# Performance work log

Hardware: AMD Instinct MI355X
Metric: run time of the kernel (lower is better)

Reference implementation:

```python
import jax, jax.numpy as jnp
import numpy as np

N_HEAD = 16
N_KV_HEAD = 4
N_EMBD = 2048

def rotate_half(x):
    x1, x2 = jnp.split(x, 2, axis=-1)
    return jnp.concatenate([-x2, x1], axis=-1)

def rope_tables(T, k):
    # angles = 10000^(-2*i/k) for i in [0, k/2); cos/sin repeated twice along last dim
    inv = jnp.power(10000.0, -2.0 * jnp.arange(k // 2, dtype=jnp.float32) / k)
    ang = jnp.arange(T, dtype=jnp.float32)[:, None] * inv[None, :]  # [T, k/2]
    cos = jnp.tile(jnp.cos(ang), (1, 2))  # [T, k]
    sin = jnp.tile(jnp.sin(ang), (1, 2))
    return cos, sin

def setup_inputs() -> dict:
    key = jax.random.key(0)
    ks = jax.random.split(key, 5)
    B, T, D = 4, 1024, N_EMBD
    g, h = N_KV_HEAD, N_HEAD
    k = D // h
    s = 0.02
    return {
        'x': jax.random.normal(ks[0], (B, T, D), dtype=jnp.float32),
        'Wq': jax.random.normal(ks[1], (D, D), dtype=jnp.float32) * s,
        'Wk': jax.random.normal(ks[2], (D, g * k), dtype=jnp.float32) * s,
        'Wv': jax.random.normal(ks[3], (D, g * k), dtype=jnp.float32) * s,
        'Wo': jax.random.normal(ks[4], (D, D), dtype=jnp.float32) * s,
    }

def reference(x, Wq, Wk, Wv, Wo):
    B, T, D = x.shape
    h, g = N_HEAD, N_KV_HEAD
    k = D // h
    Q = (x @ Wq).reshape(B, T, h, k).transpose(0, 2, 1, 3)  # [B,h,T,k]
    K = (x @ Wk).reshape(B, T, g, k).transpose(0, 2, 1, 3)  # [B,g,T,k]
    V = (x @ Wv).reshape(B, T, g, k).transpose(0, 2, 1, 3)
    # GQA: repeat_interleave kv heads to match query heads
    K = jnp.repeat(K, h // g, axis=1)  # [B,h,T,k]
    V = jnp.repeat(V, h // g, axis=1)
    cos, sin = rope_tables(T, k)
    cos = cos[None, None]  # [1,1,T,k]
    sin = sin[None, None]
    Q = Q * cos + rotate_half(Q) * sin
    K = K * cos + rotate_half(K) * sin
    scores = jnp.einsum('bhqk,bhsk->bhqs', Q, K) / jnp.sqrt(jnp.float32(k))
    causal = jnp.tril(jnp.ones((T, T), dtype=bool))
    scores = jnp.where(causal[None, None], scores, -jnp.inf)
    A = jax.nn.softmax(scores, axis=-1)
    Y = jnp.einsum('bhqs,bhsk->bhqk', A, V)
    Y = Y.transpose(0, 2, 1, 3).reshape(B, T, D)
    return Y @ Wo
```

## Files before the change

kernel.cpp:

```cpp
#include <hip/hip_runtime.h>
#include <math.h>

#define B_ 4
#define T_ 1024
#define D_ 2048
#define NH 16
#define NKV 4
#define HD 128
#define KV_D 512
#define QKV_S 2560

typedef __attribute__((ext_vector_type(8))) short short8;
typedef __attribute__((ext_vector_type(4))) float f32x4;

__device__ __forceinline__ ushort f2b(float f) {
    unsigned u = __float_as_uint(f);
    return (ushort)((u + 0x7fffu + ((u >> 16) & 1u)) >> 16);
}
__device__ __forceinline__ float b2f(ushort u) {
    return __uint_as_float((unsigned)u << 16);
}

#if __has_builtin(__builtin_amdgcn_exp2f)
#define EXP2F(x) __builtin_amdgcn_exp2f(x)
#else
#define EXP2F(x) __expf((x) * 0.6931471805599453f)
#endif

#define ASYNC_COPY16(g, l)                                                  \
    __builtin_amdgcn_global_load_lds(                                       \
        (const __attribute__((address_space(1))) void*)(g),                 \
        (__attribute__((address_space(3))) void*)(l), 16, 0, 0)

#define SCHED0() __builtin_amdgcn_sched_barrier(0)
#define SBAR() __builtin_amdgcn_s_barrier()
#define WAITV0() asm volatile("s_waitcnt vmcnt(0)" ::: "memory")
#define MFMA16(ap, bp, cc) cc = __builtin_amdgcn_mfma_f32_16x16x32_bf16(ap, bp, cc, 0, 0, 0)

__global__ __launch_bounds__(256) void prep_all(const float* __restrict__ x,
                                                const float* __restrict__ Wq,
                                                const float* __restrict__ Wk,
                                                const float* __restrict__ Wv,
                                                const float* __restrict__ Wo,
                                                ushort* __restrict__ xb,
                                                ushort* __restrict__ WqkvT,
                                                ushort* __restrict__ WoT,
                                                float2* __restrict__ tab) {
    __shared__ float tile[32][33];
    const int bid = blockIdx.x;
    if (bid < 8192) {
        const int i = bid * 256 + threadIdx.x;
        const float4 v = ((const float4*)x)[i];
        ushort4 u;
        u.x = f2b(v.x); u.y = f2b(v.y); u.z = f2b(v.z); u.w = f2b(v.w);
        ((ushort4*)xb)[i] = u;
        return;
    }
    if (bid >= 18432) {
        const int idx = (bid - 18432) * 256 + threadIdx.x;
        const int t = idx >> 6, i = idx & 63;
        const float inv = exp2f((float)i * (-13.287712379549449f / 64.0f));
        const float ang = (float)t * inv;
        tab[idx] = make_float2(cosf(ang), sinf(ang));
        return;
    }
    const float* W;
    ushort* WT;
    int N, rb;
    if (bid < 12288)      { W = Wq; WT = WqkvT;                           N = D_;   rb = bid - 8192; }
    else if (bid < 13312) { W = Wk; WT = WqkvT + (size_t)D_ * D_;         N = KV_D; rb = bid - 12288; }
    else if (bid < 14336) { W = Wv; WT = WqkvT + (size_t)(D_+KV_D) * D_;  N = KV_D; rb = bid - 13312; }
    else                  { W = Wo; WT = WoT;                             N = D_;   rb = bid - 14336; }
    const int bxn = N / 32;
    const int n0 = (rb % bxn) * 32, k0 = (rb / bxn) * 32;
    const int tx = threadIdx.x & 31, ty = threadIdx.x >> 5;
    for (int i = ty; i < 32; i += 8)
        tile[i][tx] = W[(size_t)(k0 + i) * N + n0 + tx];
    __syncthreads();
    for (int i = ty; i < 32; i += 8)
        WT[(size_t)(n0 + i) * D_ + k0 + tx] = f2b(tile[tx][i]);
}

__global__ __launch_bounds__(512, 2) void gemm_qkv256(const ushort* __restrict__ A,
                                                      const ushort* __restrict__ BT,
                                                      ushort* __restrict__ QKV,
                                                      ushort* __restrict__ Vt,
                                                      const float2* __restrict__ tab) {
    extern __shared__ ushort smem[];
    const int K = D_;
    const int NT = K / 64;
    const int tid = threadIdx.x;
    const int m0 = blockIdx.y * 256, n0 = blockIdx.x * 256;
    const int wave = tid >> 6, lane = tid & 63;
    const int wr = wave >> 2, wc = wave & 3;
    const int ln = lane & 15, quad = lane >> 4;

    const int rl = tid >> 3;
    const int cus = ((tid & 7) * 8) ^ ((rl & 7) << 3);
    const ushort* Ag = A + (size_t)(m0 + rl) * K + cus;
    const ushort* Bg = BT + (size_t)(n0 + rl) * K + cus;
    ushort* const stA = smem + tid * 8;
    ushort* const stB = smem + 32768 + tid * 8;

    const int cq0 = (quad * 8) ^ ((ln & 7) << 3);
    const int abase0 = wr * 8192 + ln * 64;
    const int bbase0 = 32768 + (wc >> 1) * 8192 + ((wc & 1) * 64 + ln) * 64;

    f32x4 acc[8][4];
    const f32x4 zero = {0.f, 0.f, 0.f, 0.f};
#pragma unroll
    for (int i = 0; i < 8; ++i)
#pragma unroll
        for (int j = 0; j < 4; ++j) acc[i][j] = zero;

    short8 a[4][2], b0[2][2], b1[2][2];

#define GLOADS(dnoff, koff)                                                 \
    do {                                                                    \
        const ushort* Agk = Ag + (koff);                                    \
        const ushort* Bgk = Bg + (koff);                                    \
        ASYNC_COPY16(Agk,                    stA + (dnoff));                \
        ASYNC_COPY16(Agk + (size_t)64 * K,   stA + (dnoff) + 4096);         \
        ASYNC_COPY16(Agk + (size_t)128 * K,  stA + (dnoff) + 8192);         \
        ASYNC_COPY16(Agk + (size_t)192 * K,  stA + (dnoff) + 12288);        \
        ASYNC_COPY16(Bgk,                    stB + (dnoff));                \
        ASYNC_COPY16(Bgk + (size_t)64 * K,   stB + (dnoff) + 4096);         \
        ASYNC_COPY16(Bgk + (size_t)128 * K,  stB + (dnoff) + 8192);         \
        ASYNC_COPY16(Bgk + (size_t)192 * K,  stB + (dnoff) + 12288);        \
    } while (0)

#define READ_A(dst, base, roff)                                             \
    _Pragma("unroll")                                                       \
    for (int mt = 0; mt < 4; ++mt) {                                        \
        dst[mt][0] = *(const short8*)&smem[(base) + (roff) + mt * 1024 + cq0];        \
        dst[mt][1] = *(const short8*)&smem[(base) + (roff) + mt * 1024 + (cq0 ^ 32)]; \
    }
#define READ_B(dst, base, noff)                                             \
    _Pragma("unroll")                                                       \
    for (int nt = 0; nt < 2; ++nt) {                                        \
        dst[nt][0] = *(const short8*)&smem[(base) + (noff) + nt * 1024 + cq0];        \
        dst[nt][1] = *(const short8*)&smem[(base) + (noff) + nt * 1024 + (cq0 ^ 32)]; \
    }
#define QUAD_MMA(ar, br, mo, no)                                            \
    _Pragma("unroll")                                                       \
    for (int mt = 0; mt < 4; ++mt)                                          \
        _Pragma("unroll")                                                   \
        for (int nt = 0; nt < 2; ++nt) {                                    \
            MFMA16(ar[mt][0], br[nt][0], acc[(mo) + mt][(no) + nt]);        \
            MFMA16(ar[mt][1], br[nt][1], acc[(mo) + mt][(no) + nt]);        \
        }

    GLOADS(0, 0);
    WAITV0();
    SBAR();
    SCHED0();
    READ_A(a, abase0, 0);
    READ_B(b0, bbase0, 0);

#pragma unroll 1
    for (int t = 0; t < NT; ++t) {
        const int cb = (t & 1) * 16384;
        const int nb = cb ^ 16384;
        const bool more = (t + 1) < NT;

        READ_B(b1, bbase0 + cb, 2048);
        if (more) GLOADS(nb, (t + 1) * 64);
        SCHED0();
        SBAR();
        __builtin_amdgcn_s_setprio(1);
        QUAD_MMA(a, b0, 0, 0);
        __builtin_amdgcn_s_setprio(0);

        SCHED0();
        SBAR();
        __builtin_amdgcn_s_setprio(1);
        QUAD_MMA(a, b1, 0, 2);
        __builtin_amdgcn_s_setprio(0);

        READ_A(a, abase0 + cb, 4096);
        __builtin_amdgcn_s_setprio(1);
        QUAD_MMA(a, b1, 4, 2);
        __builtin_amdgcn_s_setprio(0);

        if (more) WAITV0();
        SCHED0();
        SBAR();
        SCHED0();
        __builtin_amdgcn_s_setprio(1);
        QUAD_MMA(a, b0, 4, 0);
        __builtin_amdgcn_s_setprio(0);
        if (more) {
            READ_A(a, abase0 + nb, 0);
            READ_B(b0, bbase0 + nb, 0);
        }
    }
#undef GLOADS
#undef READ_A
#undef READ_B
#undef QUAD_MMA

    __syncthreads();
    ushort* Epi = smem;
    const int b = m0 >> 10;
    const int t0 = m0 & 1023;
    const int hid0 = n0 >> 7;

    for (int hh = 0; hh < 2; ++hh) {
        if ((wc >> 1) == hh) {
            const int cb2 = (wc & 1) * 64;
#pragma unroll
            for (int am = 0; am < 8; ++am)
#pragma unroll
                for (int an = 0; an < 4; ++an)
#pragma unroll
                    for (int r = 0; r < 4; ++r)
                        Epi[(wr * 128 + am * 16 + quad * 4 + r) * 136 + cb2 + an * 16 + ln] =
                            f2b(acc[am][an][r]);
        }
        __syncthreads();

        const int hid = hid0 + hh;
        if (hid < NH + NKV) {
            const bool isQ = hid < NH;
            const size_t colbase = isQ ? (size_t)hid * HD : (size_t)D_ + (size_t)(hid - NH) * HD;
            const float sc = isQ ? (0.08838834764831845f * 1.4426950408889634f) : 1.0f;
            const int r = tid >> 1;
            const int hf = tid & 1;
            const int tt = t0 + r;
            ushort* orow = QKV + (size_t)(m0 + r) * QKV_S + colbase;
            const float4* tab4 = (const float4*)tab;
#pragma unroll
            for (int jj = 0; jj < 4; ++jj) {
                const int dbase = hf * 32 + jj * 8;
                const short8 lo = *(const short8*)&Epi[r * 136 + dbase];
                const short8 hi = *(const short8*)&Epi[r * 136 + 64 + dbase];
                ushort olo[8], ohi[8];
#pragma unroll
                for (int kq = 0; kq < 4; ++kq) {
                    const float4 cs = tab4[((tt * 64 + dbase) >> 1) + kq];
                    const float x1a = b2f(lo[2 * kq]),     x2a = b2f(hi[2 * kq]);
                    const float x1b = b2f(lo[2 * kq + 1]), x2b = b2f(hi[2 * kq + 1]);
                    olo[2 * kq]     = f2b((x1a * cs.x - x2a * cs.y) * sc);
                    ohi[2 * kq]     = f2b((x2a * cs.x + x1a * cs.y) * sc);
                    olo[2 * kq + 1] = f2b((x1b * cs.z - x2b * cs.w) * sc);
                    ohi[2 * kq + 1] = f2b((x2b * cs.z + x1b * cs.w) * sc);
                }
                *(short8*)&orow[dbase]      = *(short8*)olo;
                *(short8*)&orow[dbase + 64] = *(short8*)ohi;
            }
        } else {
            const int kv = hid - (NH + NKV);
            const int dd = tid & 127;
            const int th = tid >> 7;
            ushort* vrow = Vt + ((size_t)((b * NKV + kv) * HD + dd)) * T_ + t0 + th * 64;
#pragma unroll
            for (int jj = 0; jj < 8; ++jj) {
                ushort pk[8];
#pragma unroll
                for (int k2 = 0; k2 < 8; ++k2)
                    pk[k2] = Epi[(th * 64 + jj * 8 + k2) * 136 + dd];
                *(short8*)&vrow[jj * 8] = *(short8*)pk;
            }
        }
        __syncthreads();
    }
}

__global__ __launch_bounds__(256) void gemm_bf16(const ushort* __restrict__ A,
                                                 const ushort* __restrict__ BT,
                                                 float* __restrict__ C,
                                                 int M, int N, int K) {
    __shared__ ushort As[128 * 32];
    __shared__ ushort Bs[128 * 32];
    const int tid = threadIdx.x;
    const int m0 = blockIdx.y * 128, n0 = blockIdx.x * 128;
    const int wave = tid >> 6, lane = tid & 63;
    const int wm = (wave >> 1) * 64, wn = (wave & 1) * 64;
    const int lrow = lane & 15;
    const int quad = lane >> 4;

    f32x4 acc[4][4];
    const f32x4 zero = {0.f, 0.f, 0.f, 0.f};
#pragma unroll
    for (int i = 0; i < 4; ++i)
#pragma unroll
        for (int j = 0; j < 4; ++j) acc[i][j] = zero;

    const int srow = tid >> 2;
    const int scol = (tid & 3) * 8;
    const ushort* Ag = A + (size_t)(m0 + srow) * K + scol;
    const ushort* Bg = BT + (size_t)(n0 + srow) * K + scol;
    ushort* AsT = As + tid * 8;
    ushort* BsT = Bs + tid * 8;

    for (int k0 = 0; k0 < K; k0 += 32) {
        ASYNC_COPY16(Ag + k0, AsT);
        ASYNC_COPY16(Ag + k0 + (size_t)64 * K, AsT + 64 * 32);
        ASYNC_COPY16(Bg + k0, BsT);
        ASYNC_COPY16(Bg + k0 + (size_t)64 * K, BsT + 64 * 32);
        __syncthreads();

        short8 a[4], b[4];
#pragma unroll
        for (int mt = 0; mt < 4; ++mt)
            a[mt] = *(const short8*)&As[(wm + mt * 16 + lrow) * 32 + quad * 8];
#pragma unroll
        for (int nt = 0; nt < 4; ++nt)
            b[nt] = *(const short8*)&Bs[(wn + nt * 16 + lrow) * 32 + quad * 8];
#pragma unroll
        for (int mt = 0; mt < 4; ++mt)
#pragma unroll
            for (int nt = 0; nt < 4; ++nt)
                acc[mt][nt] = __builtin_amdgcn_mfma_f32_16x16x32_bf16(
                    a[mt], b[nt], acc[mt][nt], 0, 0, 0);
        __syncthreads();
    }

    const int crow = quad * 4;
    const int ccol = lrow;
#pragma unroll
    for (int mt = 0; mt < 4; ++mt)
#pragma unroll
        for (int nt = 0; nt < 4; ++nt)
#pragma unroll
            for (int r = 0; r < 4; ++r)
                C[(size_t)(m0 + wm + mt * 16 + crow + r) * N +
                  n0 + wn + nt * 16 + ccol] = acc[mt][nt][r];
}

__global__ __launch_bounds__(256) void attn_mfma(const ushort* __restrict__ QKV,
                                                 const ushort* __restrict__ Vt,
                                                 ushort* __restrict__ Yb) {
    __shared__ ushort Ks[64][136];
    __shared__ ushort Vs[128][72];
    __shared__ ushort Ps[4][16][72];

    const int bh = blockIdx.x;
    const int qt = (int)gridDim.y - 1 - (int)blockIdx.y;
    const int b = bh >> 4, h = bh & 15;
    const int kvh = h >> 2;
    const int q0 = qt * 64;
    const int tid = threadIdx.x;
    const int wave = tid >> 6, lane = tid & 63;
    const int ln = lane & 15, quad = lane >> 4;

    short8 qf[4];
    {
        const ushort* qp = QKV + ((size_t)(b * T_ + q0 + wave * 16 + ln)) * QKV_S + h * HD + quad * 8;
#pragma unroll
        for (int f = 0; f < 4; ++f) qf[f] = *(const short8*)(qp + f * 32);
    }

    f32x4 acc[8];
    const f32x4 zero = {0.f, 0.f, 0.f, 0.f};
#pragma unroll
    for (int j = 0; j < 8; ++j) acc[j] = zero;
    float m_r[4], l_r[4];
#pragma unroll
    for (int r = 0; r < 4; ++r) { m_r[r] = -INFINITY; l_r[r] = 0.f; }

    const int qrow = q0 + wave * 16 + quad * 4;

    for (int kt = 0; kt <= qt; ++kt) {
        const int s0 = kt * 64;
        __syncthreads();
#pragma unroll
        for (int c = 0; c < 4; ++c) {
            const int cid = tid + 256 * c;
            const int s = cid >> 4, ch = cid & 15;
            *(short8*)&Ks[s][ch * 8] =
                *(const short8*)&QKV[((size_t)(b * T_ + s0 + s)) * QKV_S + D_ + kvh * HD + ch * 8];
        }
#pragma unroll
        for (int c = 0; c < 4; ++c) {
            const int cid = tid + 256 * c;
            const int d = cid >> 3, ch = cid & 7;
            *(short8*)&Vs[d][ch * 8] =
                *(const short8*)&Vt[((size_t)((b * NKV + kvh) * HD + d)) * T_ + s0 + ch * 8];
        }
        __syncthreads();

        float sc[4][4];
#pragma unroll
        for (int ct = 0; ct < 4; ++ct) {
            f32x4 s4 = zero;
#pragma unroll
            for (int f = 0; f < 4; ++f)
                s4 = __builtin_amdgcn_mfma_f32_16x16x32_bf16(
                    qf[f], *(const short8*)&Ks[ct * 16 + ln][f * 32 + quad * 8], s4, 0, 0, 0);
#pragma unroll
            for (int r = 0; r < 4; ++r) sc[ct][r] = s4[r];
        }
        if (kt == qt) {
#pragma unroll
            for (int ct = 0; ct < 4; ++ct)
#pragma unroll
                for (int r = 0; r < 4; ++r)
                    if (s0 + ct * 16 + ln > qrow + r) sc[ct][r] = -INFINITY;
        }
        float alpha[4];
#pragma unroll
        for (int r = 0; r < 4; ++r) {
            float mx = fmaxf(fmaxf(sc[0][r], sc[1][r]), fmaxf(sc[2][r], sc[3][r]));
            mx = fmaxf(mx, __shfl_xor(mx, 1));
            mx = fmaxf(mx, __shfl_xor(mx, 2));
            mx = fmaxf(mx, __shfl_xor(mx, 4));
            mx = fmaxf(mx, __shfl_xor(mx, 8));
            const float mnew = fmaxf(m_r[r], mx);
            alpha[r] = EXP2F(m_r[r] - mnew);
            m_r[r] = mnew;
#pragma unroll
            for (int ct = 0; ct < 4; ++ct) sc[ct][r] = EXP2F(sc[ct][r] - mnew);
            float sum = (sc[0][r] + sc[1][r]) + (sc[2][r] + sc[3][r]);
            sum += __shfl_xor(sum, 1);
            sum += __shfl_xor(sum, 2);
            sum += __shfl_xor(sum, 4);
            sum += __shfl_xor(sum, 8);
            l_r[r] = l_r[r] * alpha[r] + sum;
        }
#pragma unroll
        for (int ct = 0; ct < 4; ++ct)
#pragma unroll
            for (int r = 0; r < 4; ++r)
                Ps[wave][quad * 4 + r][ct * 16 + ln] = f2b(sc[ct][r]);
#pragma unroll
        for (int j = 0; j < 8; ++j)
#pragma unroll
            for (int r = 0; r < 4; ++r) acc[j][r] *= alpha[r];
        const short8 pa0 = *(const short8*)&Ps[wave][ln][quad * 8];
        const short8 pa1 = *(const short8*)&Ps[wave][ln][32 + quad * 8];
#pragma unroll
        for (int j = 0; j < 8; ++j) {
            acc[j] = __builtin_amdgcn_mfma_f32_16x16x32_bf16(
                pa0, *(const short8*)&Vs[j * 16 + ln][quad * 8], acc[j], 0, 0, 0);
            acc[j] = __builtin_amdgcn_mfma_f32_16x16x32_bf16(
                pa1, *(const short8*)&Vs[j * 16 + ln][32 + quad * 8], acc[j], 0, 0, 0);
        }
    }

    float invl[4];
#pragma unroll
    for (int r = 0; r < 4; ++r) invl[r] = 1.f / l_r[r];
    ushort* yb = Yb + ((size_t)(b * T_ + qrow)) * D_ + h * HD + ln;
#pragma unroll
    for (int r = 0; r < 4; ++r)
#pragma unroll
        for (int j = 0; j < 8; ++j)
            yb[(size_t)r * D_ + j * 16] = f2b(acc[j][r] * invl[r]);
}

extern "C" void kernel_launch(void* const* d_in, const int* in_sizes, int n_in,
                              void* d_out, int out_size, void* d_ws, size_t ws_size,
                              hipStream_t stream) {
    const float* x  = (const float*)d_in[0];
    const float* Wq = (const float*)d_in[1];
    const float* Wk = (const float*)d_in[2];
    const float* Wv = (const float*)d_in[3];
    const float* Wo = (const float*)d_in[4];
    float* out = (float*)d_out;

    char* w = (char*)d_ws;
    ushort* xb    = (ushort*)w;  w += (size_t)4096 * D_ * 2;
    ushort* WqkvT = (ushort*)w;  w += (size_t)3072 * D_ * 2;
    ushort* QKV   = (ushort*)w;  w += (size_t)4096 * QKV_S * 2;
    ushort* Vt    = (ushort*)w;  w += (size_t)B_ * KV_D * T_ * 2;
    ushort* Yb    = (ushort*)w;  w += (size_t)4096 * D_ * 2;
    ushort* WoT   = (ushort*)w;  w += (size_t)D_ * D_ * 2;
    float2* tab   = (float2*)w;  w += (size_t)T_ * 64 * 8;

    const int M = B_ * T_;
    dim3 blk(256);

    hipFuncSetAttribute(reinterpret_cast<const void*>(gemm_qkv256),
                        hipFuncAttributeMaxDynamicSharedMemorySize, 131072);

    prep_all<<<18688, blk, 0, stream>>>(x, Wq, Wk, Wv, Wo, xb, WqkvT, WoT, tab);

    gemm_qkv256<<<dim3(3072 / 256, M / 256), dim3(512), 131072, stream>>>(xb, WqkvT, QKV, Vt, tab);

    attn_mfma<<<dim3(B_ * NH, T_ / 64), blk, 0, stream>>>(QKV, Vt, Yb);

    gemm_bf16<<<dim3(D_ / 128, M / 128), blk, 0, stream>>>(Yb, WoT, out, M, D_, D_);
}
```

Measured before the change: 302.5 us.

## Deepen GEMM global-to-LDS prefetch to two tiles ahead with partial vmcnt waits

Restructures the QKV GEMM main loop so global-to-LDS async copies are issued two K-tiles ahead instead of one, using a partial vmcnt wait so the current tile can be consumed while the next is still in flight. LDS reads for a tile now happen at the top of the iteration, and the buffer is refilled after an lgkmcnt wait and a barrier once all waves have read it. This aims to hide global memory latency better and cut barriers per iteration from three to two. The cost is reliance on the vmcnt count matching the number of loads per GLOADS, plus less register-level prefetch of A/B fragments across iterations.

```diff
diff --git a/kernel.cpp b/kernel.cpp
--- a/kernel.cpp
+++ b/kernel.cpp
@@ -34,7 +34,12 @@
 
 #define SCHED0() __builtin_amdgcn_sched_barrier(0)
 #define SBAR() __builtin_amdgcn_s_barrier()
-#define WAITV0() asm volatile("s_waitcnt vmcnt(0)" ::: "memory")
+#define WAITVN(n) asm volatile("s_waitcnt vmcnt(" #n ")" ::: "memory")
+#define LGKM0()                                                             \
+    do {                                                                    \
+        asm volatile("s_waitcnt lgkmcnt(0)" ::: "memory");                  \
+        __builtin_amdgcn_sched_barrier(0);                                  \
+    } while (0)
 #define MFMA16(ap, bp, cc) cc = __builtin_amdgcn_mfma_f32_16x16x32_bf16(ap, bp, cc, 0, 0, 0)
 
 __global__ __launch_bounds__(256) void prep_all(const float* __restrict__ x,
@@ -151,48 +156,34 @@
         }
 
     GLOADS(0, 0);
-    WAITV0();
-    SBAR();
-    SCHED0();
-    READ_A(a, abase0, 0);
-    READ_B(b0, bbase0, 0);
+    GLOADS(16384, 64);
 
 #pragma unroll 1
     for (int t = 0; t < NT; ++t) {
         const int cb = (t & 1) * 16384;
-        const int nb = cb ^ 16384;
-        const bool more = (t + 1) < NT;
-
+
+        if (t + 1 < NT) { WAITVN(8); } else { WAITVN(0); }
+        SBAR();
+        SCHED0();
+
+        READ_A(a, abase0 + cb, 0);
+        READ_B(b0, bbase0 + cb, 0);
         READ_B(b1, bbase0 + cb, 2048);
-        if (more) GLOADS(nb, (t + 1) * 64);
-        SCHED0();
-        SBAR();
+
         __builtin_amdgcn_s_setprio(1);
         QUAD_MMA(a, b0, 0, 0);
-        __builtin_amdgcn_s_setprio(0);
-
-        SCHED0();
-        SBAR();
-        __builtin_amdgcn_s_setprio(1);
         QUAD_MMA(a, b1, 0, 2);
         __builtin_amdgcn_s_setprio(0);
 
         READ_A(a, abase0 + cb, 4096);
+        LGKM0();
+        SBAR();
+        if (t + 2 < NT) GLOADS(cb, (t + 2) * 64);
+        SCHED0();
         __builtin_amdgcn_s_setprio(1);
         QUAD_MMA(a, b1, 4, 2);
-        __builtin_amdgcn_s_setprio(0);
-
-        if (more) WAITV0();
-        SCHED0();
-        SBAR();
-        SCHED0();
-        __builtin_amdgcn_s_setprio(1);
         QUAD_MMA(a, b0, 4, 0);
         __builtin_amdgcn_s_setprio(0);
-        if (more) {
-            READ_A(a, abase0 + nb, 0);
-            READ_B(b0, bbase0 + nb, 0);
-        }
     }
 #undef GLOADS
 #undef READ_A
```

Result: no change. 301.4 us (-0.4%).
